# Kernel optimization log

Hardware: AMD Instinct MI355X
Metric: run time of the kernel (lower is better)

## Reference

```python
import jax, jax.numpy as jnp
import numpy as np

WS = 8      # window size
HEADS = 8

def setup_inputs() -> dict:
    key = jax.random.key(0)
    ks = jax.random.split(key, 8)
    b, dim, H, W = 128, 224, 32, 32
    inner = 224  # dim_head(28) * heads(8)
    n_win = (H // WS) * (W // WS)  # 16, matches seq_l2
    return {
        "x": jax.random.normal(ks[0], (b, dim, H, W), dtype=jnp.float32),
        "Wq": jax.random.normal(ks[1], (dim, inner), dtype=jnp.float32) * 0.02,
        "Wk": jax.random.normal(ks[2], (dim, inner), dtype=jnp.float32) * 0.02,
        "Wv": jax.random.normal(ks[3], (dim, inner), dtype=jnp.float32) * 0.02,
        "Wo": jax.random.normal(ks[4], (inner, dim), dtype=jnp.float32) * 0.02,
        "bo": jax.random.normal(ks[5], (dim,), dtype=jnp.float32) * 0.02,
        "pos_emb": jax.random.normal(ks[6], (1, 1, HEADS, n_win, n_win), dtype=jnp.float32),
        "scale": jnp.ones((1,), dtype=jnp.float32),
    }

def _forward(x, Wq, Wk, Wv, Wo, bo, pos_emb, scale):
    b, c, H, W = x.shape
    nh, nw = H // WS, W // WS
    n = nh * nw            # number of windows (attention length)
    m = WS * WS            # positions inside a window
    inner = Wq.shape[1]
    d = inner // HEADS

    xh = x.transpose(0, 2, 3, 1)                       # [b,H,W,c]
    q = xh @ Wq
    k = xh @ Wk
    v = xh @ Wv                                        # [b,H,W,inner]

    def win(t):
        # b (nh ws) (nw ws) c -> b m h n d  (attend across windows per in-window pos)
        t = t.reshape(b, nh, WS, nw, WS, inner)
        t = t.transpose(0, 1, 3, 2, 4, 5).reshape(b, n, m, inner)
        t = t.transpose(0, 2, 1, 3)                    # [b,m,n,inner]
        t = t.reshape(b, m, n, HEADS, d).transpose(0, 1, 3, 2, 4)
        return t                                       # [b,m,h,n,d]

    q2, k2, v2 = win(q), win(k), win(v)
    q2 = q2 * scale
    sim = jnp.einsum('bmhid,bmhjd->bmhij', q2, k2) + pos_emb  # [b,m,h,n,n]
    attn = jax.nn.softmax(sim, axis=-1)
    o = jnp.einsum('bmhij,bmhjd->bmhid', attn, v2)     # [b,m,h,n,d]

    o = o.transpose(0, 1, 3, 2, 4).reshape(b, m, n, inner)  # b m n (h d)
    o = o.transpose(0, 2, 1, 3)                        # [b,n,m,inner]
    o = o @ Wo + bo                                    # [b,n,m,c]
    o = o.reshape(b, nh, nw, WS, WS, c).transpose(0, 1, 3, 2, 4, 5)
    o = o.reshape(b, H, W, c)
    return o.transpose(0, 3, 1, 2)                     # [b,c,H,W]

def reference(x, Wq, Wk, Wv, Wo, bo, pos_emb, scale):
    return _forward(x, Wq, Wk, Wv, Wo, bo, pos_emb, scale)
```

## Files before the change

kernel.cpp:

```cpp
#include <hip/hip_runtime.h>
#include <stdint.h>

#define NB   128
#define CC   224
#define NWIN 16
#define DH   28
#define NHEADS 8

using bf16x8 = __attribute__((ext_vector_type(8))) short;
using u16x4  = __attribute__((ext_vector_type(4))) unsigned short;
using f32x4  = __attribute__((ext_vector_type(4))) float;

__device__ inline unsigned short f2bf(float f) {
    union { float f; unsigned u; } v; v.f = f;
    unsigned u = v.u;
    u += 0x7fffu + ((u >> 16) & 1u);
    return (unsigned short)(u >> 16);
}

__global__ void prep_weights(const float* __restrict__ Wq, const float* __restrict__ Wk,
                             const float* __restrict__ Wv, const float* __restrict__ Wo,
                             unsigned short* __restrict__ wt) {
    int e = blockIdx.x * blockDim.x + threadIdx.x;
    if (e >= 4 * CC * CC) return;
    int c   = e >> 9;
    int r   = e & 511;
    int l   = r >> 3, j = r & 7;
    int kk  = c % 7;
    int t   = c / 7;
    int sel = t / 14, ntl = t % 14;
    int n = ntl * 16 + (l & 15);
    int k = kk * 32 + (l >> 4) * 8 + j;
    const float* W = (sel == 0) ? Wq : (sel == 1) ? Wk : (sel == 2) ? Wv : Wo;
    wt[e] = f2bf(W[k * CC + n]);
}

#define QS_OFF   0
#define XS_OFF   14848
#define KS_OFF   32768
#define ATT_OFF  47616
#define SMEM_BYTES 52736

__global__ void __launch_bounds__(512, 6) attn_fused(
    const float* __restrict__ x, const unsigned short* __restrict__ wt,
    const float* __restrict__ bo, const float* __restrict__ pos,
    const float* __restrict__ scale, float* __restrict__ out)
{
    extern __shared__ char smem[];
    unsigned short* qs   = (unsigned short*)(smem + QS_OFF);
    unsigned short* xs   = (unsigned short*)(smem + XS_OFF);
    unsigned short* ks   = (unsigned short*)(smem + KS_OFF);
    unsigned short* att  = (unsigned short*)(smem + ATT_OFF);
    unsigned short* vt   = xs;
    unsigned short* ob   = qs;
    float*          oout = (float*)(smem + XS_OFF);

    const int tid = threadIdx.x;
    const int wv  = tid >> 6;
    const int l   = tid & 63;
    const int g   = l >> 4;
    const int li  = l & 15;

    const int bid = blockIdx.x;
    const int xcd = bid & 7;
    const int idx = bid >> 3;
    const int hq  = idx & 3;
    const int wg  = (xcd << 7) + (idx >> 2);
    const int bi  = wg >> 3;
    const int mr  = wg & 7;

    {
        const float* xb = x + ((size_t)bi * CC << 10);
        for (int q = tid; q < CC * NWIN; q += 512) {
            int ch = q >> 4, wx = q & 15;
            int wi = wx >> 2, wj = wx & 3;
            int h = wi * 8 + mr, w0 = wj * 8 + hq * 2;
            float2 v2 = *(const float2*)(xb + (ch << 10) + (h << 5) + w0);
            xs[wx * 232 + ch]        = f2bf(v2.x);
            xs[(wx + 16) * 232 + ch] = f2bf(v2.y);
        }
    }
    const float scl = scale[0];
    __syncthreads();

    const int mt = wv & 1;
    const int arow = mt * 16 + li;
    bf16x8 a1f[7];
    #pragma unroll
    for (int kk = 0; kk < 7; ++kk)
        a1f[kk] = *(const bf16x8*)(xs + arow * 232 + kk * 32 + g * 8);
    __syncthreads();

    for (int d = wv >> 1; d < 21; d += 4) {
        int t0 = 2 * d;
        int sel = t0 / 14, ntl0 = t0 % 14;
        const unsigned short* w0 = wt + (size_t)t0 * 3584 + l * 8;
        f32x4 acc0 = {0.f, 0.f, 0.f, 0.f}, acc1 = {0.f, 0.f, 0.f, 0.f};
        #pragma unroll
        for (int kk = 0; kk < 7; ++kk) {
            bf16x8 bf0 = *(const bf16x8*)(w0 + kk * 512);
            bf16x8 bf1 = *(const bf16x8*)(w0 + 3584 + kk * 512);
            acc0 = __builtin_amdgcn_mfma_f32_16x16x32_bf16(a1f[kk], bf0, acc0, 0, 0, 0);
            acc1 = __builtin_amdgcn_mfma_f32_16x16x32_bf16(a1f[kk], bf1, acc1, 0, 0, 0);
        }
        int colb = ntl0 * 16 + li;
        #pragma unroll
        for (int r = 0; r < 4; ++r) {
            int row = mt * 16 + g * 4 + r;
            float v0 = acc0[r], v1 = acc1[r];
            if (sel == 0) {
                qs[row * 232 + colb]      = f2bf(v0 * scl);
                qs[row * 232 + colb + 16] = f2bf(v1 * scl);
            } else if (sel == 1) {
                ks[row * 232 + colb]      = f2bf(v0);
                ks[row * 232 + colb + 16] = f2bf(v1);
            } else {
                vt[colb * 40 + row]        = f2bf(v0);
                vt[(colb + 16) * 40 + row] = f2bf(v1);
            }
        }
    }
    __syncthreads();

    const int hd = wv;
    const int cb = hd * DH;
    float pv4[4];
    #pragma unroll
    for (int r = 0; r < 4; ++r)
        pv4[r] = pos[(hd * 16 + g * 4 + r) * 16 + li];
    f32x4 sim[2];
    #pragma unroll
    for (int mc2 = 0; mc2 < 2; ++mc2) {
        int rowq = li + mc2 * 16;
        bf16x8 aq, bk;
        const unsigned short* qp = qs + rowq * 232 + cb + g * 8;
        const unsigned short* kp = ks + rowq * 232 + cb + g * 8;
        u16x4 qlo = *(const u16x4*)qp, qhi = *(const u16x4*)(qp + 4);
        u16x4 klo = *(const u16x4*)kp, khi = *(const u16x4*)(kp + 4);
        if (g == 3) { qhi = (u16x4)0; khi = (u16x4)0; }
        #pragma unroll
        for (int j = 0; j < 4; ++j) {
            aq[j] = (short)qlo[j]; aq[4 + j] = (short)qhi[j];
            bk[j] = (short)klo[j]; bk[4 + j] = (short)khi[j];
        }
        f32x4 z = {0.f, 0.f, 0.f, 0.f};
        sim[mc2] = __builtin_amdgcn_mfma_f32_16x16x32_bf16(aq, bk, z, 0, 0, 0);
    }
    __syncthreads();

    {
        unsigned short* attw0 = att + wv * 320;
        unsigned short* attw1 = ks  + wv * 320;
        bf16x8 bv00, bv01, bv10, bv11;
        if (g < 2) {
            bv00 = *(const bf16x8*)(vt + (cb + li) * 40      + g * 8);
            bv01 = *(const bf16x8*)(vt + (cb + 16 + li) * 40 + g * 8);
            bv10 = *(const bf16x8*)(vt + (cb + li) * 40      + 16 + g * 8);
            bv11 = *(const bf16x8*)(vt + (cb + 16 + li) * 40 + 16 + g * 8);
        } else {
            bv00 = (bf16x8)0; bv01 = (bf16x8)0; bv10 = (bf16x8)0; bv11 = (bf16x8)0;
        }
        float ev[2][4];
        #pragma unroll
        for (int mc2 = 0; mc2 < 2; ++mc2)
            #pragma unroll
            for (int r = 0; r < 4; ++r)
                ev[mc2][r] = __expf(sim[mc2][r] + pv4[r]);
        #pragma unroll
        for (int mc2 = 0; mc2 < 2; ++mc2) {
            unsigned short* aw = mc2 ? attw1 : attw0;
            #pragma unroll
            for (int r = 0; r < 4; ++r) {
                float sm = ev[mc2][r];
                sm += __shfl_xor(sm, 1, 16);
                sm += __shfl_xor(sm, 2, 16);
                sm += __shfl_xor(sm, 4, 16);
                sm += __shfl_xor(sm, 8, 16);
                aw[(g * 4 + r) * 20 + li] = f2bf(ev[mc2][r] * __builtin_amdgcn_rcpf(sm));
            }
        }
        bf16x8 pa0 = (bf16x8)0, pa1 = (bf16x8)0;
        if (g < 2) {
            const unsigned short* ap0 = attw0 + li * 20 + g * 8;
            const unsigned short* ap1 = attw1 + li * 20 + g * 8;
            u16x4 a0lo = *(const u16x4*)ap0, a0hi = *(const u16x4*)(ap0 + 4);
            u16x4 a1lo = *(const u16x4*)ap1, a1hi = *(const u16x4*)(ap1 + 4);
            #pragma unroll
            for (int j = 0; j < 4; ++j) {
                pa0[j] = (short)a0lo[j]; pa0[4 + j] = (short)a0hi[j];
                pa1[j] = (short)a1lo[j]; pa1[4 + j] = (short)a1hi[j];
            }
        }
        f32x4 z00 = {0.f,0.f,0.f,0.f}, z01 = {0.f,0.f,0.f,0.f};
        f32x4 z10 = {0.f,0.f,0.f,0.f}, z11 = {0.f,0.f,0.f,0.f};
        f32x4 po00 = __builtin_amdgcn_mfma_f32_16x16x32_bf16(pa0, bv00, z00, 0, 0, 0);
        f32x4 po10 = __builtin_amdgcn_mfma_f32_16x16x32_bf16(pa1, bv10, z10, 0, 0, 0);
        f32x4 po01 = __builtin_amdgcn_mfma_f32_16x16x32_bf16(pa0, bv01, z01, 0, 0, 0);
        f32x4 po11 = __builtin_amdgcn_mfma_f32_16x16x32_bf16(pa1, bv11, z11, 0, 0, 0);
        int dh0 = li;
        int dh1 = 16 + li;
        #pragma unroll
        for (int r = 0; r < 4; ++r) {
            int i = g * 4 + r;
            ob[i * 232 + cb + dh0]        = f2bf(po00[r]);
            ob[(i + 16) * 232 + cb + dh0] = f2bf(po10[r]);
        }
        if (dh1 < DH) {
            #pragma unroll
            for (int r = 0; r < 4; ++r) {
                int i = g * 4 + r;
                ob[i * 232 + cb + dh1]        = f2bf(po01[r]);
                ob[(i + 16) * 232 + cb + dh1] = f2bf(po11[r]);
            }
        }
    }
    __syncthreads();

    bf16x8 a3f[7];
    #pragma unroll
    for (int kk = 0; kk < 7; ++kk)
        a3f[kk] = *(const bf16x8*)(ob + arow * 232 + kk * 32 + g * 8);

    for (int d = wv >> 1; d < 7; d += 4) {
        int t0 = 2 * d;
        const unsigned short* w0 = wt + (size_t)(42 + t0) * 3584 + l * 8;
        f32x4 acc0 = {0.f, 0.f, 0.f, 0.f}, acc1 = {0.f, 0.f, 0.f, 0.f};
        #pragma unroll
        for (int kk = 0; kk < 7; ++kk) {
            bf16x8 bf0 = *(const bf16x8*)(w0 + kk * 512);
            bf16x8 bf1 = *(const bf16x8*)(w0 + 3584 + kk * 512);
            acc0 = __builtin_amdgcn_mfma_f32_16x16x32_bf16(a3f[kk], bf0, acc0, 0, 0, 0);
            acc1 = __builtin_amdgcn_mfma_f32_16x16x32_bf16(a3f[kk], bf1, acc1, 0, 0, 0);
        }
        int colb = t0 * 16 + li;
        #pragma unroll
        for (int r = 0; r < 4; ++r) {
            int row = mt * 16 + g * 4 + r;
            oout[row * 225 + colb]      = acc0[r];
            oout[row * 225 + colb + 16] = acc1[r];
        }
    }
    __syncthreads();

    {
        float* outb = out + ((size_t)bi * CC << 10);
        for (int q = tid; q < CC * NWIN; q += 512) {
            int ch = q >> 4, wx = q & 15;
            int wi = wx >> 2, wj = wx & 3;
            int h = wi * 8 + mr, w0 = wj * 8 + hq * 2;
            float b = bo[ch];
            float2 v2;
            v2.x = oout[wx * 225 + ch] + b;
            v2.y = oout[(wx + 16) * 225 + ch] + b;
            *(float2*)(outb + (ch << 10) + (h << 5) + w0) = v2;
        }
    }
}

extern "C" void kernel_launch(void* const* d_in, const int* in_sizes, int n_in,
                              void* d_out, int out_size, void* d_ws, size_t ws_size,
                              hipStream_t stream) {
    const float* x   = (const float*)d_in[0];
    const float* Wq  = (const float*)d_in[1];
    const float* Wk  = (const float*)d_in[2];
    const float* Wv  = (const float*)d_in[3];
    const float* Wo  = (const float*)d_in[4];
    const float* bo  = (const float*)d_in[5];
    const float* pos = (const float*)d_in[6];
    const float* scl = (const float*)d_in[7];
    float* out = (float*)d_out;
    unsigned short* wt = (unsigned short*)d_ws;

    prep_weights<<<dim3((4 * CC * CC + 255) / 256), dim3(256), 0, stream>>>(Wq, Wk, Wv, Wo, wt);

    (void)hipFuncSetAttribute((const void*)attn_fused,
                              hipFuncAttributeMaxDynamicSharedMemorySize, SMEM_BYTES);
    attn_fused<<<dim3(NB * 8 * 4), dim3(512), SMEM_BYTES, stream>>>(x, wt, bo, pos, scl, out);
}
```

Baseline: 145.8 us.

## Process two batch items per block and prefetch the next item's input into registers

```diff
diff --git a/kernel.cpp b/kernel.cpp
--- a/kernel.cpp
+++ b/kernel.cpp
@@ -66,193 +66,225 @@
     const int idx = bid >> 3;
     const int hq  = idx & 3;
     const int wg  = (xcd << 7) + (idx >> 2);
-    const int bi  = wg >> 3;
+    const int bi0 = wg >> 3;
     const int mr  = wg & 7;
 
-    {
-        const float* xb = x + ((size_t)bi * CC << 10);
-        for (int q = tid; q < CC * NWIN; q += 512) {
-            int ch = q >> 4, wx = q & 15;
-            int wi = wx >> 2, wj = wx & 3;
-            int h = wi * 8 + mr, w0 = wj * 8 + hq * 2;
-            float2 v2 = *(const float2*)(xb + (ch << 10) + (h << 5) + w0);
-            xs[wx * 232 + ch]        = f2bf(v2.x);
-            xs[(wx + 16) * 232 + ch] = f2bf(v2.y);
-        }
-    }
-    const float scl = scale[0];
-    __syncthreads();
-
-    const int mt = wv & 1;
-    const int arow = mt * 16 + li;
-    bf16x8 a1f[7];
+    float2 xpre[7];
+    float  scl = 0.f;
+    float  pv4[4];
+
     #pragma unroll
-    for (int kk = 0; kk < 7; ++kk)
-        a1f[kk] = *(const bf16x8*)(xs + arow * 232 + kk * 32 + g * 8);
-    __syncthreads();
-
-    for (int d = wv >> 1; d < 21; d += 4) {
-        int t0 = 2 * d;
-        int sel = t0 / 14, ntl0 = t0 % 14;
-        const unsigned short* w0 = wt + (size_t)t0 * 3584 + l * 8;
-        f32x4 acc0 = {0.f, 0.f, 0.f, 0.f}, acc1 = {0.f, 0.f, 0.f, 0.f};
+    for (int item = 0; item < 2; ++item) {
+        const int bi = bi0 + (item << 3);
+
+        if (item) __syncthreads();
+
+        if (item == 0) {
+            const float* xb = x + ((size_t)bi * CC << 10);
+            for (int q = tid; q < CC * NWIN; q += 512) {
+                int ch = q >> 4, wx = q & 15;
+                int wi = wx >> 2, wj = wx & 3;
+                int h = wi * 8 + mr, w0 = wj * 8 + hq * 2;
+                float2 v2 = *(const float2*)(xb + (ch << 10) + (h << 5) + w0);
+                xs[wx * 232 + ch]        = f2bf(v2.x);
+                xs[(wx + 16) * 232 + ch] = f2bf(v2.y);
+            }
+            scl = scale[0];
+        } else {
+            #pragma unroll
+            for (int it = 0; it < 7; ++it) {
+                int q = tid + 512 * it;
+                int ch = q >> 4, wx = q & 15;
+                xs[wx * 232 + ch]        = f2bf(xpre[it].x);
+                xs[(wx + 16) * 232 + ch] = f2bf(xpre[it].y);
+            }
+        }
+        __syncthreads();
+
+        const int mt = wv & 1;
+        const int arow = mt * 16 + li;
+        bf16x8 a1f[7];
         #pragma unroll
-        for (int kk = 0; kk < 7; ++kk) {
-            bf16x8 bf0 = *(const bf16x8*)(w0 + kk * 512);
-            bf16x8 bf1 = *(const bf16x8*)(w0 + 3584 + kk * 512);
-            acc0 = __builtin_amdgcn_mfma_f32_16x16x32_bf16(a1f[kk], bf0, acc0, 0, 0, 0);
-            acc1 = __builtin_amdgcn_mfma_f32_16x16x32_bf16(a1f[kk], bf1, acc1, 0, 0, 0);
-        }
-        int colb = ntl0 * 16 + li;
-        #pragma unroll
-        for (int r = 0; r < 4; ++r) {
-            int row = mt * 16 + g * 4 + r;
-            float v0 = acc0[r], v1 = acc1[r];
-            if (sel == 0) {
-                qs[row * 232 + colb]      = f2bf(v0 * scl);
-                qs[row * 232 + colb + 16] = f2bf(v1 * scl);
-            } else if (sel == 1) {
-                ks[row * 232 + colb]      = f2bf(v0);
-                ks[row * 232 + colb + 16] = f2bf(v1);
-            } else {
-                vt[colb * 40 + row]        = f2bf(v0);
-                vt[(colb + 16) * 40 + row] = f2bf(v1);
-            }
-        }
-    }
-    __syncthreads();
-
-    const int hd = wv;
-    const int cb = hd * DH;
-    float pv4[4];
-    #pragma unroll
-    for (int r = 0; r < 4; ++r)
-        pv4[r] = pos[(hd * 16 + g * 4 + r) * 16 + li];
-    f32x4 sim[2];
-    #pragma unroll
-    for (int mc2 = 0; mc2 < 2; ++mc2) {
-        int rowq = li + mc2 * 16;
-        bf16x8 aq, bk;
-        const unsigned short* qp = qs + rowq * 232 + cb + g * 8;
-        const unsigned short* kp = ks + rowq * 232 + cb + g * 8;
-        u16x4 qlo = *(const u16x4*)qp, qhi = *(const u16x4*)(qp + 4);
-        u16x4 klo = *(const u16x4*)kp, khi = *(const u16x4*)(kp + 4);
-        if (g == 3) { qhi = (u16x4)0; khi = (u16x4)0; }
-        #pragma unroll
-        for (int j = 0; j < 4; ++j) {
-            aq[j] = (short)qlo[j]; aq[4 + j] = (short)qhi[j];
-            bk[j] = (short)klo[j]; bk[4 + j] = (short)khi[j];
-        }
-        f32x4 z = {0.f, 0.f, 0.f, 0.f};
-        sim[mc2] = __builtin_amdgcn_mfma_f32_16x16x32_bf16(aq, bk, z, 0, 0, 0);
-    }
-    __syncthreads();
-
-    {
-        unsigned short* attw0 = att + wv * 320;
-        unsigned short* attw1 = ks  + wv * 320;
-        bf16x8 bv00, bv01, bv10, bv11;
-        if (g < 2) {
-            bv00 = *(const bf16x8*)(vt + (cb + li) * 40      + g * 8);
-            bv01 = *(const bf16x8*)(vt + (cb + 16 + li) * 40 + g * 8);
-            bv10 = *(const bf16x8*)(vt + (cb + li) * 40      + 16 + g * 8);
-            bv11 = *(const bf16x8*)(vt + (cb + 16 + li) * 40 + 16 + g * 8);
-        } else {
-            bv00 = (bf16x8)0; bv01 = (bf16x8)0; bv10 = (bf16x8)0; bv11 = (bf16x8)0;
-        }
-        float ev[2][4];
-        #pragma unroll
-        for (int mc2 = 0; mc2 < 2; ++mc2)
+        for (int kk = 0; kk < 7; ++kk)
+            a1f[kk] = *(const bf16x8*)(xs + arow * 232 + kk * 32 + g * 8);
+
+        if (item == 0) {
+            const float* xb1 = x + ((size_t)(bi0 + 8) * CC << 10);
+            #pragma unroll
+            for (int it = 0; it < 7; ++it) {
+                int q = tid + 512 * it;
+                int ch = q >> 4, wx = q & 15;
+                int wi = wx >> 2, wj = wx & 3;
+                int h = wi * 8 + mr, w0 = wj * 8 + hq * 2;
+                xpre[it] = *(const float2*)(xb1 + (ch << 10) + (h << 5) + w0);
+            }
+        }
+        __syncthreads();
+
+        for (int d = wv >> 1; d < 21; d += 4) {
+            int t0 = 2 * d;
+            int sel = t0 / 14, ntl0 = t0 % 14;
+            const unsigned short* w0 = wt + (size_t)t0 * 3584 + l * 8;
+            f32x4 acc0 = {0.f, 0.f, 0.f, 0.f}, acc1 = {0.f, 0.f, 0.f, 0.f};
+            #pragma unroll
+            for (int kk = 0; kk < 7; ++kk) {
+                bf16x8 bf0 = *(const bf16x8*)(w0 + kk * 512);
+                bf16x8 bf1 = *(const bf16x8*)(w0 + 3584 + kk * 512);
+                acc0 = __builtin_amdgcn_mfma_f32_16x16x32_bf16(a1f[kk], bf0, acc0, 0, 0, 0);
+                acc1 = __builtin_amdgcn_mfma_f32_16x16x32_bf16(a1f[kk], bf1, acc1, 0, 0, 0);
+            }
+            int colb = ntl0 * 16 + li;
+            #pragma unroll
+            for (int r = 0; r < 4; ++r) {
+                int row = mt * 16 + g * 4 + r;
+                float v0 = acc0[r], v1 = acc1[r];
+                if (sel == 0) {
+                    qs[row * 232 + colb]      = f2bf(v0 * scl);
+                    qs[row * 232 + colb + 16] = f2bf(v1 * scl);
+                } else if (sel == 1) {
+                    ks[row * 232 + colb]      = f2bf(v0);
+                    ks[row * 232 + colb + 16] = f2bf(v1);
+                } else {
+                    vt[colb * 40 + row]        = f2bf(v0);
+                    vt[(colb + 16) * 40 + row] = f2bf(v1);
+                }
+            }
+        }
+        __syncthreads();
+
+        const int hd = wv;
+        const int cb = hd * DH;
+        if (item == 0) {
             #pragma unroll
             for (int r = 0; r < 4; ++r)
-                ev[mc2][r] = __expf(sim[mc2][r] + pv4[r]);
+                pv4[r] = pos[(hd * 16 + g * 4 + r) * 16 + li];
+        }
+        f32x4 sim[2];
         #pragma unroll
         for (int mc2 = 0; mc2 < 2; ++mc2) {
-            unsigned short* aw = mc2 ? attw1 : attw0;
-            #pragma unroll
-            for (int r = 0; r < 4; ++r) {
-                float sm = ev[mc2][r];
-                sm += __shfl_xor(sm, 1, 16);
-                sm += __shfl_xor(sm, 2, 16);
-                sm += __shfl_xor(sm, 4, 16);
-                sm += __shfl_xor(sm, 8, 16);
-                aw[(g * 4 + r) * 20 + li] = f2bf(ev[mc2][r] * __builtin_amdgcn_rcpf(sm));
-            }
-        }
-        bf16x8 pa0 = (bf16x8)0, pa1 = (bf16x8)0;
-        if (g < 2) {
-            const unsigned short* ap0 = attw0 + li * 20 + g * 8;
-            const unsigned short* ap1 = attw1 + li * 20 + g * 8;
-            u16x4 a0lo = *(const u16x4*)ap0, a0hi = *(const u16x4*)(ap0 + 4);
-            u16x4 a1lo = *(const u16x4*)ap1, a1hi = *(const u16x4*)(ap1 + 4);
+            int rowq = li + mc2 * 16;
+            bf16x8 aq, bk;
+            const unsigned short* qp = qs + rowq * 232 + cb + g * 8;
+            const unsigned short* kp = ks + rowq * 232 + cb + g * 8;
+            u16x4 qlo = *(const u16x4*)qp, qhi = *(const u16x4*)(qp + 4);
+            u16x4 klo = *(const u16x4*)kp, khi = *(const u16x4*)(kp + 4);
+            if (g == 3) { qhi = (u16x4)0; khi = (u16x4)0; }
             #pragma unroll
             for (int j = 0; j < 4; ++j) {
-                pa0[j] = (short)a0lo[j]; pa0[4 + j] = (short)a0hi[j];
-                pa1[j] = (short)a1lo[j]; pa1[4 + j] = (short)a1hi[j];
-            }
-        }
-        f32x4 z00 = {0.f,0.f,0.f,0.f}, z01 = {0.f,0.f,0.f,0.f};
-        f32x4 z10 = {0.f,0.f,0.f,0.f}, z11 = {0.f,0.f,0.f,0.f};
-        f32x4 po00 = __builtin_amdgcn_mfma_f32_16x16x32_bf16(pa0, bv00, z00, 0, 0, 0);
-        f32x4 po10 = __builtin_amdgcn_mfma_f32_16x16x32_bf16(pa1, bv10, z10, 0, 0, 0);
-        f32x4 po01 = __builtin_amdgcn_mfma_f32_16x16x32_bf16(pa0, bv01, z01, 0, 0, 0);
-        f32x4 po11 = __builtin_amdgcn_mfma_f32_16x16x32_bf16(pa1, bv11, z11, 0, 0, 0);
-        int dh0 = li;
-        int dh1 = 16 + li;
-        #pragma unroll
-        for (int r = 0; r < 4; ++r) {
-            int i = g * 4 + r;
-            ob[i * 232 + cb + dh0]        = f2bf(po00[r]);
-            ob[(i + 16) * 232 + cb + dh0] = f2bf(po10[r]);
-        }
-        if (dh1 < DH) {
+                aq[j] = (short)qlo[j]; aq[4 + j] = (short)qhi[j];
+                bk[j] = (short)klo[j]; bk[4 + j] = (short)khi[j];
+            }
+            f32x4 z = {0.f, 0.f, 0.f, 0.f};
+            sim[mc2] = __builtin_amdgcn_mfma_f32_16x16x32_bf16(aq, bk, z, 0, 0, 0);
+        }
+        __syncthreads();
+
+        {
+            unsigned short* attw0 = att + wv * 320;
+            unsigned short* attw1 = ks  + wv * 320;
+            bf16x8 bv00, bv01, bv10, bv11;
+            if (g < 2) {
+                bv00 = *(const bf16x8*)(vt + (cb + li) * 40      + g * 8);
+                bv01 = *(const bf16x8*)(vt + (cb + 16 + li) * 40 + g * 8);
+                bv10 = *(const bf16x8*)(vt + (cb + li) * 40      + 16 + g * 8);
+                bv11 = *(const bf16x8*)(vt + (cb + 16 + li) * 40 + 16 + g * 8);
+            } else {
+                bv00 = (bf16x8)0; bv01 = (bf16x8)0; bv10 = (bf16x8)0; bv11 = (bf16x8)0;
+            }
+            float ev[2][4];
+            #pragma unroll
+            for (int mc2 = 0; mc2 < 2; ++mc2)
+                #pragma unroll
+                for (int r = 0; r < 4; ++r)
+                    ev[mc2][r] = __expf(sim[mc2][r] + pv4[r]);
+            #pragma unroll
+            for (int mc2 = 0; mc2 < 2; ++mc2) {
+                unsigned short* aw = mc2 ? attw1 : attw0;
+                #pragma unroll
+                for (int r = 0; r < 4; ++r) {
+                    float sm = ev[mc2][r];
+                    sm += __shfl_xor(sm, 1, 16);
+                    sm += __shfl_xor(sm, 2, 16);
+                    sm += __shfl_xor(sm, 4, 16);
+                    sm += __shfl_xor(sm, 8, 16);
+                    aw[(g * 4 + r) * 20 + li] = f2bf(ev[mc2][r] * __builtin_amdgcn_rcpf(sm));
+                }
+            }
+            bf16x8 pa0 = (bf16x8)0, pa1 = (bf16x8)0;
+            if (g < 2) {
+                const unsigned short* ap0 = attw0 + li * 20 + g * 8;
+                const unsigned short* ap1 = attw1 + li * 20 + g * 8;
+                u16x4 a0lo = *(const u16x4*)ap0, a0hi = *(const u16x4*)(ap0 + 4);
+                u16x4 a1lo = *(const u16x4*)ap1, a1hi = *(const u16x4*)(ap1 + 4);
+                #pragma unroll
+                for (int j = 0; j < 4; ++j) {
+                    pa0[j] = (short)a0lo[j]; pa0[4 + j] = (short)a0hi[j];
+                    pa1[j] = (short)a1lo[j]; pa1[4 + j] = (short)a1hi[j];
+                }
+            }
+            f32x4 z00 = {0.f,0.f,0.f,0.f}, z01 = {0.f,0.f,0.f,0.f};
+            f32x4 z10 = {0.f,0.f,0.f,0.f}, z11 = {0.f,0.f,0.f,0.f};
+            f32x4 po00 = __builtin_amdgcn_mfma_f32_16x16x32_bf16(pa0, bv00, z00, 0, 0, 0);
+            f32x4 po10 = __builtin_amdgcn_mfma_f32_16x16x32_bf16(pa1, bv10, z10, 0, 0, 0);
+            f32x4 po01 = __builtin_amdgcn_mfma_f32_16x16x32_bf16(pa0, bv01, z01, 0, 0, 0);
+            f32x4 po11 = __builtin_amdgcn_mfma_f32_16x16x32_bf16(pa1, bv11, z11, 0, 0, 0);
+            int dh0 = li;
+            int dh1 = 16 + li;
             #pragma unroll
             for (int r = 0; r < 4; ++r) {
                 int i = g * 4 + r;
-                ob[i * 232 + cb + dh1]        = f2bf(po01[r]);
-                ob[(i + 16) * 232 + cb + dh1] = f2bf(po11[r]);
-            }
-        }
-    }
-    __syncthreads();
-
-    bf16x8 a3f[7];
-    #pragma unroll
-    for (int kk = 0; kk < 7; ++kk)
-        a3f[kk] = *(const bf16x8*)(ob + arow * 232 + kk * 32 + g * 8);
-
-    for (int d = wv >> 1; d < 7; d += 4) {
-        int t0 = 2 * d;
-        const unsigned short* w0 = wt + (size_t)(42 + t0) * 3584 + l * 8;
-        f32x4 acc0 = {0.f, 0.f, 0.f, 0.f}, acc1 = {0.f, 0.f, 0.f, 0.f};
+                ob[i * 232 + cb + dh0]        = f2bf(po00[r]);
+                ob[(i + 16) * 232 + cb + dh0] = f2bf(po10[r]);
+            }
+            if (dh1 < DH) {
+                #pragma unroll
+                for (int r = 0; r < 4; ++r) {
+                    int i = g * 4 + r;
+                    ob[i * 232 + cb + dh1]        = f2bf(po01[r]);
+                    ob[(i + 16) * 232 + cb + dh1] = f2bf(po11[r]);
+                }
+            }
+        }
+        __syncthreads();
+
+        bf16x8 a3f[7];
         #pragma unroll
-        for (int kk = 0; kk < 7; ++kk) {
-            bf16x8 bf0 = *(const bf16x8*)(w0 + kk * 512);
-            bf16x8 bf1 = *(const bf16x8*)(w0 + 3584 + kk * 512);
-            acc0 = __builtin_amdgcn_mfma_f32_16x16x32_bf16(a3f[kk], bf0, acc0, 0, 0, 0);
-            acc1 = __builtin_amdgcn_mfma_f32_16x16x32_bf16(a3f[kk], bf1, acc1, 0, 0, 0);
-        }
-        int colb = t0 * 16 + li;
-        #pragma unroll
-        for (int r = 0; r < 4; ++r) {
-            int row = mt * 16 + g * 4 + r;
-            oout[row * 225 + colb]      = acc0[r];
-            oout[row * 225 + colb + 16] = acc1[r];
-        }
-    }
-    __syncthreads();
-
-    {
-        float* outb = out + ((size_t)bi * CC << 10);
-        for (int q = tid; q < CC * NWIN; q += 512) {
-            int ch = q >> 4, wx = q & 15;
-            int wi = wx >> 2, wj = wx & 3;
-            int h = wi * 8 + mr, w0 = wj * 8 + hq * 2;
-            float b = bo[ch];
-            float2 v2;
-            v2.x = oout[wx * 225 + ch] + b;
-            v2.y = oout[(wx + 16) * 225 + ch] + b;
-            *(float2*)(outb + (ch << 10) + (h << 5) + w0) = v2;
+        for (int kk = 0; kk < 7; ++kk)
+            a3f[kk] = *(const bf16x8*)(ob + arow * 232 + kk * 32 + g * 8);
+
+        for (int d = wv >> 1; d < 7; d += 4) {
+            int t0 = 2 * d;
+            const unsigned short* w0 = wt + (size_t)(42 + t0) * 3584 + l * 8;
+            f32x4 acc0 = {0.f, 0.f, 0.f, 0.f}, acc1 = {0.f, 0.f, 0.f, 0.f};
+            #pragma unroll
+            for (int kk = 0; kk < 7; ++kk) {
+                bf16x8 bf0 = *(const bf16x8*)(w0 + kk * 512);
+                bf16x8 bf1 = *(const bf16x8*)(w0 + 3584 + kk * 512);
+                acc0 = __builtin_amdgcn_mfma_f32_16x16x32_bf16(a3f[kk], bf0, acc0, 0, 0, 0);
+                acc1 = __builtin_amdgcn_mfma_f32_16x16x32_bf16(a3f[kk], bf1, acc1, 0, 0, 0);
+            }
+            int colb = t0 * 16 + li;
+            #pragma unroll
+            for (int r = 0; r < 4; ++r) {
+                int row = mt * 16 + g * 4 + r;
+                oout[row * 225 + colb]      = acc0[r];
+                oout[row * 225 + colb + 16] = acc1[r];
+            }
+        }
+        __syncthreads();
+
+        {
+            float* outb = out + ((size_t)bi * CC << 10);
+            for (int q = tid; q < CC * NWIN; q += 512) {
+                int ch = q >> 4, wx = q & 15;
+                int wi = wx >> 2, wj = wx & 3;
+                int h = wi * 8 + mr, w0 = wj * 8 + hq * 2;
+                float b = bo[ch];
+                float2 v2;
+                v2.x = oout[wx * 225 + ch] + b;
+                v2.y = oout[(wx + 16) * 225 + ch] + b;
+                *(float2*)(outb + (ch << 10) + (h << 5) + w0) = v2;
+            }
         }
     }
 }
@@ -275,5 +307,5 @@
 
     (void)hipFuncSetAttribute((const void*)attn_fused,
                               hipFuncAttributeMaxDynamicSharedMemorySize, SMEM_BYTES);
-    attn_fused<<<dim3(NB * 8 * 4), dim3(512), SMEM_BYTES, stream>>>(x, wt, bo, pos, scl, out);
+    attn_fused<<<dim3(NB * 8 * 2), dim3(512), SMEM_BYTES, stream>>>(x, wt, bo, pos, scl, out);
 }
```

After: 201.3 us. +38.1%, slower.
